# Kernel optimization log

Measured on AMD Instinct MI355X. Metric: run time of the kernel, lower is better.

## Reference

```python
import jax, jax.numpy as jnp
import numpy as np

B, H, S, D = 2, 8, 2048, 64
N_HASHES = 6
EPS = 1e-8


def setup_inputs() -> dict:
    key = jax.random.key(0)
    kq, kk, kv, kr = jax.random.split(key, 4)
    Q = jax.random.normal(kq, (B, H, S, D), dtype=jnp.float32)
    K = jax.random.normal(kk, (B, H, S, D), dtype=jnp.float32)
    V = jax.random.normal(kv, (B, H, S, D), dtype=jnp.float32)
    rotations = jax.random.normal(kr, (H, N_HASHES, D), dtype=jnp.float32)
    return {"Q": Q, "K": K, "V": V, "rotations": rotations}


def _buckets(X, rotations, powers):
    # X: [b,h,l,d] -> integer bucket id per position, [b,h,l]
    Xn = X / (jnp.linalg.norm(X, axis=-1, keepdims=True) + 1e-8)
    bits = jnp.einsum('bhld,hnd->bhln', Xn, rotations) > 0
    return jnp.sum(bits.astype(jnp.int32) * powers, axis=-1)


def reference(Q, K, V, rotations):
    n_hashes = rotations.shape[1]
    d = Q.shape[-1]
    powers = (2 ** jnp.arange(n_hashes)).astype(jnp.int32)
    q_buckets = _buckets(Q, rotations, powers)  # [b,h,sq]
    k_buckets = _buckets(K, rotations, powers)  # [b,h,sk]
    # queries only attend to keys whose full hash code matches exactly
    match = q_buckets[..., :, None] == k_buckets[..., None, :]  # [b,h,sq,sk]
    scores = jnp.einsum('bhqd,bhkd->bhqk', Q, K) / (d ** 0.5)
    row_has = jnp.any(match, axis=-1, keepdims=True)
    masked = jnp.where(match, scores, -jnp.inf)
    m = jnp.max(masked, axis=-1, keepdims=True)
    m = jnp.where(row_has, m, 0.0)  # avoid -inf for empty rows
    e = jnp.where(match, jnp.exp(scores - m), 0.0)
    weights = e / (jnp.sum(e, axis=-1, keepdims=True) + EPS)
    out = jnp.einsum('bhqk,bhkd->bhqd', weights, V)
    return out / n_hashes
```

## Files before the change

kernel.cpp:

```cpp
#include <hip/hip_runtime.h>
#include <math.h>


constexpr int S_LEN = 2048;
constexpr int D = 64;
constexpr int NHASH = 6;
constexpr int BH = 16;
constexpr int NB = 64;
constexpr int QPAD = 4;
constexpr int PADQ = S_LEN + (QPAD - 1) * NB;
constexpr int NGRP = PADQ / QPAD;
constexpr int NBLK = NGRP / 4;
constexpr int KCH = 32;

__global__ __launch_bounds__(256) void lsh_buckets2(const float* __restrict__ Q,
                                                    const float* __restrict__ K,
                                                    const float* __restrict__ rot,
                                                    int* __restrict__ qb,
                                                    int* __restrict__ kb) {
    const int gw   = (blockIdx.x * 256 + threadIdx.x) >> 6;
    const int lane = threadIdx.x & 63;
    const bool isK = gw >= BH * S_LEN;
    const int wid  = isK ? gw - BH * S_LEN : gw;
    const float* X = isK ? K : Q;
    int* dst       = isK ? kb : qb;
    const int h    = (wid >> 11) & 7;

    const float x  = X[(size_t)wid * D + lane];
    const float* r = rot + (size_t)h * NHASH * D + lane;
    float p0 = x * r[0 * D], p1 = x * r[1 * D], p2 = x * r[2 * D];
    float p3 = x * r[3 * D], p4 = x * r[4 * D], p5 = x * r[5 * D];
#pragma unroll
    for (int off = 32; off >= 1; off >>= 1) {
        p0 += __shfl_xor(p0, off, 64);
        p1 += __shfl_xor(p1, off, 64);
        p2 += __shfl_xor(p2, off, 64);
        p3 += __shfl_xor(p3, off, 64);
        p4 += __shfl_xor(p4, off, 64);
        p5 += __shfl_xor(p5, off, 64);
    }
    int bucket = (p0 > 0.f ? 1 : 0) | (p1 > 0.f ? 2 : 0) | (p2 > 0.f ? 4 : 0) |
                 (p3 > 0.f ? 8 : 0) | (p4 > 0.f ? 16 : 0) | (p5 > 0.f ? 32 : 0);
    if (lane == 0) dst[wid] = bucket;
}

__global__ __launch_bounds__(256) void lsh_count_scan(const int* __restrict__ qbuckets,
                                                      const int* __restrict__ kbuckets,
                                                      int* __restrict__ kstart_packed,
                                                      int* __restrict__ cur_q,
                                                      int* __restrict__ cur_k) {
    __shared__ int hist[NB];
    const int which = blockIdx.x >> 4;
    const int bh    = blockIdx.x & 15;
    const int tid   = threadIdx.x;
    const int* src  = (which ? kbuckets : qbuckets) + bh * S_LEN;

    if (tid < NB) hist[tid] = 0;
    __syncthreads();
#pragma unroll
    for (int i = 0; i < 8; ++i)
        atomicAdd(&hist[src[i * 256 + tid]], 1);
    __syncthreads();

    if (tid < 64) {
        const int cnt = hist[tid];
        const int v   = which ? cnt : ((cnt + QPAD - 1) & ~(QPAD - 1));
        int x = v;
#pragma unroll
        for (int off = 1; off < 64; off <<= 1) {
            const int y = __shfl_up(x, off, 64);
            if (tid >= off) x += y;
        }
        const int start = x - v;
        if (which) {
            kstart_packed[bh * NB + tid] = start | (cnt << 16);
            cur_k[bh * NB + tid] = start;
        } else {
            cur_q[bh * NB + tid] = start;
        }
    }
}

__global__ __launch_bounds__(256) void lsh_place(const int* __restrict__ qbuckets,
                                                 const int* __restrict__ kbuckets,
                                                 int* __restrict__ cur_q,
                                                 int* __restrict__ cur_k,
                                                 int* __restrict__ q_plist,
                                                 int* __restrict__ k_list) {
    const int gw    = blockIdx.x * 256 + threadIdx.x;
    const int which = gw >> 15;
    const int idx   = gw & (BH * S_LEN - 1);
    const int bh    = idx >> 11;
    const int i     = idx & (S_LEN - 1);
    if (which) {
        const int b    = kbuckets[idx];
        const int slot = atomicAdd(&cur_k[bh * NB + b], 1);
        k_list[bh * S_LEN + slot] = i;
    } else {
        const int b    = qbuckets[idx];
        const int slot = atomicAdd(&cur_q[bh * NB + b], 1);
        q_plist[bh * PADQ + slot] = i | (b << 16);
    }
}

__global__ __launch_bounds__(256) void lsh_attn_d(const float* __restrict__ Q,
                                                  const float* __restrict__ K,
                                                  const float* __restrict__ V,
                                                  const int* __restrict__ q_plist,
                                                  const int* __restrict__ kstart_packed,
                                                  const int* __restrict__ k_list,
                                                  float* __restrict__ out) {
    __shared__ float qlds[4][QPAD][64];
    __shared__ float wbuf[4][QPAD][KCH];
    __shared__ int   kbuf[4][KCH];

    const int wv   = threadIdx.x >> 6;
    const int lane = threadIdx.x & 63;
    const int h    = lane >> 5;
    const int kk   = lane & 31;
    const int bh   = blockIdx.y;
    const int grp  = blockIdx.x + wv * NBLK;

    const int4 dqv = *(const int4*)(q_plist + bh * PADQ + 4 * grp);
    const int e0 = __builtin_amdgcn_readfirstlane(dqv.x);
    if (e0 < 0) return;
    const int bucket = e0 >> 16;
    const int e1 = __builtin_amdgcn_readfirstlane(dqv.y);
    const int e2 = __builtin_amdgcn_readfirstlane(dqv.z);
    const int e3 = __builtin_amdgcn_readfirstlane(dqv.w);
    const int ksnk = __builtin_amdgcn_readfirstlane(kstart_packed[bh * NB + bucket]);
    const int ks = ksnk & 0xFFFF;
    const int nk = ksnk >> 16;

    const int q0 = e0 & 0xFFFF;
    const bool v1 = e1 >= 0, v2 = e2 >= 0, v3 = e3 >= 0;
    const int q1 = v1 ? (e1 & 0xFFFF) : q0;
    const int q2 = v2 ? (e2 & 0xFFFF) : q0;
    const int q3 = v3 ? (e3 & 0xFFFF) : q0;

    float* outb = out + (size_t)bh * S_LEN * D;
    if (nk == 0) {
        outb[(size_t)q0 * D + lane] = 0.0f;
        if (v1) outb[(size_t)q1 * D + lane] = 0.0f;
        if (v2) outb[(size_t)q2 * D + lane] = 0.0f;
        if (v3) outb[(size_t)q3 * D + lane] = 0.0f;
        return;
    }

    const int* kl   = k_list + bh * S_LEN + ks;
    const float* Kb = K + (size_t)bh * S_LEN * D;
    const float* Vb = V + (size_t)bh * S_LEN * D;
    const float* Qb = Q + (size_t)bh * S_LEN * D;

    qlds[wv][0][lane] = Qb[(size_t)q0 * D + lane];
    qlds[wv][1][lane] = Qb[(size_t)q1 * D + lane];
    qlds[wv][2][lane] = Qb[(size_t)q2 * D + lane];
    qlds[wv][3][lane] = Qb[(size_t)q3 * D + lane];

    float l0 = 0.f, l1 = 0.f;
    float acc[QPAD] = {0.f, 0.f, 0.f, 0.f};

    for (int c = 0; c * KCH < nk; ++c) {
        const int cnk  = min(KCH, nk - c * KCH);
        const int kidx = kl[c * KCH + min(kk, cnk - 1)];
        const float* krow = Kb + (size_t)kidx * D + h * 32;

        float4 kv[8];
#pragma unroll
        for (int i = 0; i < 8; ++i) kv[i] = *(const float4*)(krow + i * 4);

        float s[QPAD];
#pragma unroll
        for (int j = 0; j < QPAD; ++j) {
            const float* qj = &qlds[wv][j][h * 32];
            float sj = 0.f;
#pragma unroll
            for (int i = 0; i < 8; ++i) {
                const float4 qv = *(const float4*)(qj + i * 4);
                sj += qv.x * kv[i].x + qv.y * kv[i].y + qv.z * kv[i].z + qv.w * kv[i].w;
            }
            s[j] = sj;
        }
        s[0] += __shfl_xor(s[0], 32, 64);
        s[1] += __shfl_xor(s[1], 32, 64);
        s[2] += __shfl_xor(s[2], 32, 64);
        s[3] += __shfl_xor(s[3], 32, 64);

        const bool kvalid = kk < cnk;
        const float sa = h ? s[2] : s[0];
        const float sb = h ? s[3] : s[1];
        const float ea = kvalid ? __expf(sa * 0.125f) : 0.f;
        const float eb = kvalid ? __expf(sb * 0.125f) : 0.f;
        l0 += ea;
        l1 += eb;
        wbuf[wv][2 * h + 0][kk] = ea;
        wbuf[wv][2 * h + 1][kk] = eb;
        if (h == 0) kbuf[wv][kk] = kidx;

        const int ng = (cnk + 3) >> 2;
        for (int g = 0; g < ng; ++g) {
            const int4 kx = *(const int4*)&kbuf[wv][g * 4];
            const float vx = Vb[(size_t)kx.x * D + lane];
            const float vy = Vb[(size_t)kx.y * D + lane];
            const float vz = Vb[(size_t)kx.z * D + lane];
            const float vw = Vb[(size_t)kx.w * D + lane];
            const float4 eA = *(const float4*)&wbuf[wv][0][g * 4];
            const float4 eB = *(const float4*)&wbuf[wv][1][g * 4];
            const float4 eC = *(const float4*)&wbuf[wv][2][g * 4];
            const float4 eD = *(const float4*)&wbuf[wv][3][g * 4];
            acc[0] += eA.x * vx + eA.y * vy + eA.z * vz + eA.w * vw;
            acc[1] += eB.x * vx + eB.y * vy + eB.z * vz + eB.w * vw;
            acc[2] += eC.x * vx + eC.y * vy + eC.z * vz + eC.w * vw;
            acc[3] += eD.x * vx + eD.y * vy + eD.z * vz + eD.w * vw;
        }
    }

#pragma unroll
    for (int off = 16; off >= 1; off >>= 1) {
        l0 += __shfl_xor(l0, off, 64);
        l1 += __shfl_xor(l1, off, 64);
    }
    const float o0 = __shfl_xor(l0, 32, 64);
    const float o1 = __shfl_xor(l1, 32, 64);
    const float lq0 = h ? o0 : l0;
    const float lq1 = h ? o1 : l1;
    const float lq2 = h ? l0 : o0;
    const float lq3 = h ? l1 : o1;

    const float inv6 = 1.0f / 6.0f;
    outb[(size_t)q0 * D + lane] = acc[0] / (lq0 + 1e-8f) * inv6;
    if (v1) outb[(size_t)q1 * D + lane] = acc[1] / (lq1 + 1e-8f) * inv6;
    if (v2) outb[(size_t)q2 * D + lane] = acc[2] / (lq2 + 1e-8f) * inv6;
    if (v3) outb[(size_t)q3 * D + lane] = acc[3] / (lq3 + 1e-8f) * inv6;
}

extern "C" void kernel_launch(void* const* d_in, const int* in_sizes, int n_in,
                              void* d_out, int out_size, void* d_ws, size_t ws_size,
                              hipStream_t stream) {
    const float* Q   = (const float*)d_in[0];
    const float* K   = (const float*)d_in[1];
    const float* V   = (const float*)d_in[2];
    const float* rot = (const float*)d_in[3];
    float* out = (float*)d_out;

    char* ws = (char*)d_ws;
    int* q_buckets     = (int*)(ws);
    int* k_buckets     = (int*)(ws + 131072);
    int* k_list        = (int*)(ws + 262144);
    int* q_plist       = (int*)(ws + 393216);
    int* kstart_packed = (int*)(ws + 540672);
    int* cur_q         = (int*)(ws + 544768);
    int* cur_k         = (int*)(ws + 548864);

    lsh_buckets2<<<2 * BH * S_LEN / 4, 256, 0, stream>>>(Q, K, rot, q_buckets, k_buckets);
    lsh_count_scan<<<32, 256, 0, stream>>>(q_buckets, k_buckets, kstart_packed, cur_q, cur_k);
    hipMemsetAsync(q_plist, 0xFF, BH * PADQ * sizeof(int), stream);
    lsh_place<<<2 * BH * S_LEN / 256, 256, 0, stream>>>(q_buckets, k_buckets, cur_q, cur_k,
                                                        q_plist, k_list);
    lsh_attn_d<<<dim3(NBLK, BH), 256, 0, stream>>>(Q, K, V, q_plist, kstart_packed,
                                                   k_list, out);
}
```

Before: 83.46 us.

## Fuse bucket count, scan and placement into one kernel, drop memset

Merges the histogram/scan kernel, the memset of the padded query list, and the placement kernel into one kernel per (which, bh) block. Scatter uses shared-memory atomics instead of global atomics, and padding slots are filled with -1 explicitly. This removes two launches and a memset, but the fused kernel runs on only 32 blocks. The attention kernel also changes its group-to-wave mapping to consecutive groups and loads the plist as scalars instead of an int4.

Measured after the change: 73.46 us. 12.0% less time.

```diff
diff --git a/kernel.cpp b/kernel.cpp
--- a/kernel.cpp
+++ b/kernel.cpp
@@ -44,12 +44,15 @@
     if (lane == 0) dst[wid] = bucket;
 }
 
-__global__ __launch_bounds__(256) void lsh_count_scan(const int* __restrict__ qbuckets,
-                                                      const int* __restrict__ kbuckets,
-                                                      int* __restrict__ kstart_packed,
-                                                      int* __restrict__ cur_q,
-                                                      int* __restrict__ cur_k) {
+__global__ __launch_bounds__(256) void lsh_sortfuse(const int* __restrict__ qbuckets,
+                                                    const int* __restrict__ kbuckets,
+                                                    int* __restrict__ q_plist,
+                                                    int* __restrict__ kstart_packed,
+                                                    int* __restrict__ k_list) {
     __shared__ int hist[NB];
+    __shared__ int start[NB];
+    __shared__ int cur[NB];
+    __shared__ int total;
     const int which = blockIdx.x >> 4;
     const int bh    = blockIdx.x & 15;
     const int tid   = threadIdx.x;
@@ -57,12 +60,16 @@
 
     if (tid < NB) hist[tid] = 0;
     __syncthreads();
-#pragma unroll
-    for (int i = 0; i < 8; ++i)
-        atomicAdd(&hist[src[i * 256 + tid]], 1);
+
+    int myb[8];
+#pragma unroll
+    for (int i = 0; i < 8; ++i) {
+        myb[i] = src[i * 256 + tid];
+        atomicAdd(&hist[myb[i]], 1);
+    }
     __syncthreads();
 
-    if (tid < 64) {
+    if (tid < NB) {
         const int cnt = hist[tid];
         const int v   = which ? cnt : ((cnt + QPAD - 1) & ~(QPAD - 1));
         int x = v;
@@ -71,35 +78,36 @@
             const int y = __shfl_up(x, off, 64);
             if (tid >= off) x += y;
         }
-        const int start = x - v;
-        if (which) {
-            kstart_packed[bh * NB + tid] = start | (cnt << 16);
-            cur_k[bh * NB + tid] = start;
-        } else {
-            cur_q[bh * NB + tid] = start;
-        }
-    }
-}
-
-__global__ __launch_bounds__(256) void lsh_place(const int* __restrict__ qbuckets,
-                                                 const int* __restrict__ kbuckets,
-                                                 int* __restrict__ cur_q,
-                                                 int* __restrict__ cur_k,
-                                                 int* __restrict__ q_plist,
-                                                 int* __restrict__ k_list) {
-    const int gw    = blockIdx.x * 256 + threadIdx.x;
-    const int which = gw >> 15;
-    const int idx   = gw & (BH * S_LEN - 1);
-    const int bh    = idx >> 11;
-    const int i     = idx & (S_LEN - 1);
-    if (which) {
-        const int b    = kbuckets[idx];
-        const int slot = atomicAdd(&cur_k[bh * NB + b], 1);
-        k_list[bh * S_LEN + slot] = i;
+        const int st = x - v;
+        start[tid] = st;
+        cur[tid]   = st;
+        if (which) kstart_packed[bh * NB + tid] = st | (cnt << 16);
+        if (tid == 63) total = x;
+    }
+    __syncthreads();
+
+    if (!which) {
+        int* qp = q_plist + bh * PADQ;
+        if (tid < NB) {
+            const int cnt    = hist[tid];
+            const int padded = (cnt + QPAD - 1) & ~(QPAD - 1);
+            for (int t = start[tid] + cnt; t < start[tid] + padded; ++t) qp[t] = -1;
+        }
+        for (int t = total + tid; t < PADQ; t += 256) qp[t] = -1;
+#pragma unroll
+        for (int i = 0; i < 8; ++i) {
+            const int b    = myb[i];
+            const int slot = atomicAdd(&cur[b], 1);
+            qp[slot] = (i * 256 + tid) | (b << 16);
+        }
     } else {
-        const int b    = qbuckets[idx];
-        const int slot = atomicAdd(&cur_q[bh * NB + b], 1);
-        q_plist[bh * PADQ + slot] = i | (b << 16);
+        int* klp = k_list + bh * S_LEN;
+#pragma unroll
+        for (int i = 0; i < 8; ++i) {
+            const int b    = myb[i];
+            const int slot = atomicAdd(&cur[b], 1);
+            klp[slot] = i * 256 + tid;
+        }
     }
 }
 
@@ -119,15 +127,15 @@
     const int h    = lane >> 5;
     const int kk   = lane & 31;
     const int bh   = blockIdx.y;
-    const int grp  = blockIdx.x + wv * NBLK;
-
-    const int4 dqv = *(const int4*)(q_plist + bh * PADQ + 4 * grp);
-    const int e0 = __builtin_amdgcn_readfirstlane(dqv.x);
+    const int grp  = blockIdx.x * 4 + wv;
+
+    const int* pl = q_plist + bh * PADQ + 4 * grp;
+    const int e0 = __builtin_amdgcn_readfirstlane(pl[0]);
     if (e0 < 0) return;
     const int bucket = e0 >> 16;
-    const int e1 = __builtin_amdgcn_readfirstlane(dqv.y);
-    const int e2 = __builtin_amdgcn_readfirstlane(dqv.z);
-    const int e3 = __builtin_amdgcn_readfirstlane(dqv.w);
+    const int e1 = __builtin_amdgcn_readfirstlane(pl[1]);
+    const int e2 = __builtin_amdgcn_readfirstlane(pl[2]);
+    const int e3 = __builtin_amdgcn_readfirstlane(pl[3]);
     const int ksnk = __builtin_amdgcn_readfirstlane(kstart_packed[bh * NB + bucket]);
     const int ks = ksnk & 0xFFFF;
     const int nk = ksnk >> 16;
@@ -249,14 +257,9 @@
     int* k_list        = (int*)(ws + 262144);
     int* q_plist       = (int*)(ws + 393216);
     int* kstart_packed = (int*)(ws + 540672);
-    int* cur_q         = (int*)(ws + 544768);
-    int* cur_k         = (int*)(ws + 548864);
 
     lsh_buckets2<<<2 * BH * S_LEN / 4, 256, 0, stream>>>(Q, K, rot, q_buckets, k_buckets);
-    lsh_count_scan<<<32, 256, 0, stream>>>(q_buckets, k_buckets, kstart_packed, cur_q, cur_k);
-    hipMemsetAsync(q_plist, 0xFF, BH * PADQ * sizeof(int), stream);
-    lsh_place<<<2 * BH * S_LEN / 256, 256, 0, stream>>>(q_buckets, k_buckets, cur_q, cur_k,
-                                                        q_plist, k_list);
+    lsh_sortfuse<<<32, 256, 0, stream>>>(q_buckets, k_buckets, q_plist, kstart_packed, k_list);
     lsh_attn_d<<<dim3(NBLK, BH), 256, 0, stream>>>(Q, K, V, q_plist, kstart_packed,
                                                    k_list, out);
 }
```
